# Kernel tuning notes

Measured on AMD Instinct MI355X. Metric: run time of the kernel, lower is better.

The kernel has to match this reference:

```python
import jax, jax.numpy as jnp
import numpy as np

TOTAL_WORDS = 10000
EMBED_LEN = 100
SEQ_LEN = 80
BATCH = 2048
UNITS = 1024


def setup_inputs() -> dict:
    key = jax.random.key(0)
    ks = jax.random.split(key, 8)
    inputs = jax.random.randint(ks[0], (BATCH, SEQ_LEN), 0, TOTAL_WORDS)
    s = 0.02
    emb = jax.random.normal(ks[1], (TOTAL_WORDS, EMBED_LEN), jnp.float32) * s
    W0 = jax.random.normal(ks[2], (EMBED_LEN, 4 * UNITS), jnp.float32) * s
    U0 = jax.random.normal(ks[3], (UNITS, 4 * UNITS), jnp.float32) * s
    b0 = jnp.zeros((4 * UNITS,), jnp.float32)
    W1 = jax.random.normal(ks[4], (UNITS, 4 * UNITS), jnp.float32) * s
    U1 = jax.random.normal(ks[5], (UNITS, 4 * UNITS), jnp.float32) * s
    b1 = jnp.zeros((4 * UNITS,), jnp.float32)
    fcW = jax.random.normal(ks[6], (UNITS, 1), jnp.float32) * s
    fcb = jnp.zeros((1,), jnp.float32)
    return {"inputs": inputs, "emb": emb, "W0": W0, "U0": U0, "b0": b0,
            "W1": W1, "U1": U1, "b1": b1, "fcW": fcW, "fcb": fcb}


def _lstm_step(x, h, c, W, U, b):
    # Keras LSTMCell gate order: i, f, g(candidate), o
    z = x @ W + h @ U + b  # [B, 4*units]
    i, f, g, o = jnp.split(z, 4, axis=-1)
    i = jax.nn.sigmoid(i)
    f = jax.nn.sigmoid(f)
    g = jnp.tanh(g)
    o = jax.nn.sigmoid(o)
    c_new = f * c + i * g
    h_new = o * jnp.tanh(c_new)
    return h_new, c_new


def reference(inputs, emb, W0, U0, b0, W1, U1, b1, fcW, fcb):
    x = emb[inputs]                      # [B, T, E]
    xs = jnp.transpose(x, (1, 0, 2))     # [T, B, E] for scan over time
    B = inputs.shape[0]
    U = U0.shape[0]
    init = (jnp.zeros((B, U), x.dtype), jnp.zeros((B, U), x.dtype),
            jnp.zeros((B, U), x.dtype), jnp.zeros((B, U), x.dtype))

    def step(carry, xt):
        h0, c0, h1, c1 = carry
        h0, c0 = _lstm_step(xt, h0, c0, W0, U0, b0)
        h1, c1 = _lstm_step(h0, h1, c1, W1, U1, b1)
        return (h0, c0, h1, c1), None

    (h0, c0, h1, c1), _ = jax.lax.scan(step, init, xs)
    logits = h1 @ fcW + fcb              # [B, 1]
    return jax.nn.sigmoid(logits)
```

## Files before the change

### kernel.cpp

```cpp
#include <hip/hip_runtime.h>

#define DEVI __device__ __forceinline__

typedef __attribute__((ext_vector_type(4))) float f4;
typedef long long i64t;

DEVI unsigned char f2fp8(float x) {
  int p = __builtin_amdgcn_cvt_pk_fp8_f32(x, x, 0, false);
  return (unsigned char)(p & 0xff);
}
DEVI float fp82f(unsigned char b) {
  return __builtin_amdgcn_cvt_f32_fp8((int)b, 0);
}
DEVI float sigmoidf_(float x) { return 1.f / (1.f + __expf(-x)); }
DEVI float tanhf_(float x) {
  float ax = fabsf(x);
  float e = __expf(-2.f * ax);
  float t = (1.f - e) / (1.f + e);
  return x < 0.f ? -t : t;
}

#define GLDS16(g, l) __builtin_amdgcn_global_load_lds( \
    (const __attribute__((address_space(1))) void*)(g), \
    (__attribute__((address_space(3))) void*)(l), 16, 0, 0)

#define SCALE_UP 64.0f
#define SCALE_DN (1.0f / 4096.0f)


__global__ void k_conv_emb(const float* __restrict__ emb, unsigned char* __restrict__ ep) {
  int i = blockIdx.x * 256 + threadIdx.x;
  if (i >= 10000 * 128) return;
  int r = i >> 7, c = i & 127;
  ep[i] = (c < 100) ? f2fp8(emb[r * 100 + c] * SCALE_UP) : (unsigned char)0;
}

DEVI int permn(int n) {
  int g = n >> 10, u = n & 1023;
  return (u >> 5) * 128 + ((u >> 4) & 1) * 64 + g * 16 + (u & 15);
}
DEVI int kswz(int klog, int row) {
  return (klog & ~63) | (((((klog >> 3) & 7) ^ ((row >> 1) & 7))) << 3) | (klog & 7);
}

__global__ void k_conv_w0(const float* __restrict__ W0, const float* __restrict__ U0,
                          unsigned char* __restrict__ WT) {
  int i = blockIdx.x * 256 + threadIdx.x;
  if (i >= 4096 * 1152) return;
  int n = i / 1152, k = i - n * 1152;
  float v;
  if (k < 100) v = W0[k * 4096 + n];
  else if (k < 128) v = 0.f;
  else v = U0[(k - 128) * 4096 + n];
  int np = permn(n);
  WT[(size_t)np * 1152 + kswz(k, np)] = f2fp8(v * SCALE_UP);
}

__global__ void k_conv_w1(const float* __restrict__ W1, const float* __restrict__ U1,
                          unsigned char* __restrict__ WT) {
  int i = blockIdx.x * 256 + threadIdx.x;
  if (i >= 4096 * 2048) return;
  int n = i >> 11, k = i & 2047;
  float v = (k < 1024) ? W1[k * 4096 + n] : U1[(k - 1024) * 4096 + n];
  int np = permn(n);
  WT[(size_t)np * 2048 + kswz(k, np)] = f2fp8(v * SCALE_UP);
}


template<int K1, int KTOT, bool GATHER>
DEVI void lstm_body(int tile, char* smem,
    const unsigned char* __restrict__ src1,
    const unsigned char* __restrict__ src2,
    const int* __restrict__ idx, int t,
    const unsigned char* __restrict__ WT,
    const float* __restrict__ bias,
    float* __restrict__ cbuf,
    unsigned char* __restrict__ hout)
{
  const int tid = threadIdx.x;
  const int bn = tile & 31;
  const int bm = tile >> 5;
  const int m0 = bm * 256;
  const int n0 = bn * 128;

  const int lr = tid >> 2;
  const int c16 = (tid & 3) * 16;
  const int csw = (((tid & 3) ^ ((tid >> 3) & 3))) * 16;

  const unsigned char* g1[2];
  if (GATHER) {
#pragma unroll
    for (int p = 0; p < 2; ++p) {
      int w = idx[(m0 + p * 128 + lr) * 80 + t];
      g1[p] = src1 + (size_t)w * K1 + csw;
    }
  }

  const unsigned char* wbase = WT + (size_t)(n0 + lr) * KTOT + c16;
  const unsigned char* a1b[2];
  const unsigned char* a2b[2];
#pragma unroll
  for (int p = 0; p < 2; ++p) {
    size_t row = (size_t)(m0 + p * 128 + lr);
    a1b[p] = src1 + row * 1024 + c16;
    a2b[p] = src2 + row * 1024 + c16 - K1;
  }

  char* const LA0 = smem;
  char* const LB0 = smem + 16384;
  char* const LA1 = smem + 24576;
  char* const LB1 = smem + 40960;

  auto stage = [&](int kb, char* la, char* lb) {
    const int kc = kb * 64;
    if (GATHER && kc < K1) {
#pragma unroll
      for (int p = 0; p < 2; ++p)
        GLDS16(g1[p] + kc, la + p * 8192 + tid * 16);
    } else {
#pragma unroll
      for (int p = 0; p < 2; ++p) {
        const unsigned char* g = (!GATHER && kc < K1) ? a1b[p] + kc
                                                      : a2b[p] + kc;
        GLDS16(g, la + p * 8192 + tid * 16);
      }
    }
    GLDS16(wbase + kc, lb + tid * 16);
  };

  const int lane = tid & 63;
  const int wv = tid >> 6;
  const int wm = wv >> 1;
  const int wn = wv & 1;
  const int cl = lane & 15;
  const int qd = lane >> 4;
  const int qh = qd >> 1, qb = qd & 1;
  const int g8s = (cl >> 1) & 7;
  const int ko8_0 = ((0 + qd) ^ g8s) << 3;
  const int ko8_1 = ((4 + qd) ^ g8s) << 3;
  const int g4s = (cl >> 1) & 3;
  const int ko16_0 = ((qh ^ g4s) << 4) + qb * 8;
  const int ko16_1 = (((2 + qh) ^ g4s) << 4) + qb * 8;

  f4 acc[4][4];
  const f4 fz = {0.f, 0.f, 0.f, 0.f};
#pragma unroll
  for (int a = 0; a < 4; ++a)
#pragma unroll
    for (int b = 0; b < 4; ++b) acc[a][b] = fz;

  auto compute = [&](char* la, char* lb, int koA0, int koA1) {
#pragma unroll
    for (int kk = 0; kk < 2; ++kk) {
      const int koA = kk ? koA1 : koA0;
      const int koB = kk ? ko8_1 : ko8_0;
      i64t af[4], bfr[4];
#pragma unroll
      for (int mi = 0; mi < 4; ++mi)
        af[mi] = *(const i64t*)(la + (wm * 64 + mi * 16 + cl) * 64 + koA);
#pragma unroll
      for (int j = 0; j < 4; ++j)
        bfr[j] = *(const i64t*)(lb + (wn * 64 + j * 16 + cl) * 64 + koB);
#pragma unroll
      for (int mi = 0; mi < 4; ++mi)
#pragma unroll
        for (int j = 0; j < 4; ++j)
          acc[mi][j] = __builtin_amdgcn_mfma_f32_16x16x32_fp8_fp8(
              af[mi], bfr[j], acc[mi][j], 0, 0, 0);
    }
  };

  stage(0, LA0, LB0);

  constexpr int NKB = KTOT / 64;
  static_assert(NKB % 2 == 0, "K-loop unroll-2 requires even NKB");
#pragma unroll 1
  for (int kbp = 0; kbp < NKB / 2; ++kbp) {
    const int kb0 = kbp * 2;
    __syncthreads();
    stage(kb0 + 1, LA1, LB1);
    {
      const bool A16 = GATHER && (kb0 * 64) < K1;
      compute(LA0, LB0, A16 ? ko16_0 : ko8_0, A16 ? ko16_1 : ko8_1);
    }
    __syncthreads();
    if (kb0 + 2 < NKB) stage(kb0 + 2, LA0, LB0);
    {
      const bool A16 = GATHER && ((kb0 + 1) * 64) < K1;
      compute(LA1, LB1, A16 ? ko16_0 : ko8_0, A16 ? ko16_1 : ko8_1);
    }
  }

  const int u = bn * 32 + wn * 16 + cl;
  const int uhi = u & ~63;
  const int uc8 = (u >> 3) & 7;
  const int ulo = u & 7;
  const float bi = bias[u];
  const float bff = bias[1024 + u];
  const float bg = bias[2048 + u];
  const float bo = bias[3072 + u];
#pragma unroll
  for (int mi = 0; mi < 4; ++mi) {
    int mbase = m0 + wm * 64 + mi * 16 + qd * 4;
#pragma unroll
    for (int r = 0; r < 4; ++r) {
      int m = mbase + r;
      int fm = (qd * 2 + (r >> 1)) & 7;
      int hcol = uhi | ((uc8 ^ fm) << 3) | ulo;
      float gi = sigmoidf_(acc[mi][0][r] * SCALE_DN + bi);
      float gf = sigmoidf_(acc[mi][1][r] * SCALE_DN + bff);
      float gg = tanhf_(acc[mi][2][r] * SCALE_DN + bg);
      float go = sigmoidf_(acc[mi][3][r] * SCALE_DN + bo);
      size_t coff = (size_t)m * 1024 + u;
      float cn = gf * cbuf[coff] + gi * gg;
      cbuf[coff] = cn;
      hout[(size_t)m * 1024 + hcol] = f2fp8(go * tanhf_(cn) * SCALE_UP);
    }
  }
}

__global__ __launch_bounds__(512, 4) void k_step(
    int mode,
    const unsigned char* embp, const unsigned char* h0in,
    const int* idx, int t,
    const unsigned char* WT0, const float* b0, float* c0, unsigned char* h0out,
    const unsigned char* h0prev, const unsigned char* h1in,
    const unsigned char* WT1, const float* b1, float* c1, unsigned char* h1out)
{
  extern __shared__ char smem[];
  const int blk = blockIdx.x;
  int tile;
  bool isL0;
  if (mode == 1) {
    int s = blk >> 3;
    isL0 = ((s & 1) ^ (s >> 5)) != 0;
    tile = (blk & 7) * 32 + (s & 31);
  } else {
    tile = (blk & 7) * 32 + (blk >> 3);
    isL0 = (mode == 0);
  }
  if (isL0)
    lstm_body<128, 1152, true>(tile, smem, embp, h0in, idx, t,
                               WT0, b0, c0, h0out);
  else
    lstm_body<1024, 2048, false>(tile, smem, h0prev, h1in, nullptr, 0,
                                 WT1, b1, c1, h1out);
}


__global__ void k_fc(const unsigned char* __restrict__ h1,
                     const float* __restrict__ fcW, const float* __restrict__ fcb,
                     float* __restrict__ out) {
  int wv = threadIdx.x >> 6;
  int lane = threadIdx.x & 63;
  int row = blockIdx.x * 4 + wv;
  if (row >= 2048) return;
  const unsigned char* hr = h1 + (size_t)row * 1024;
  const int f = (row >> 1) & 7;
  float s = 0.f;
  for (int k = lane; k < 1024; k += 64) {
    int ks = (k & ~63) | ((((k >> 3) & 7) ^ f) << 3) | (k & 7);
    s += fp82f(hr[ks]) * fcW[k];
  }
#pragma unroll
  for (int off = 32; off > 0; off >>= 1) s += __shfl_down(s, off);
  if (lane == 0) out[row] = sigmoidf_(s * (1.0f / SCALE_UP) + fcb[0]);
}


extern "C" void kernel_launch(void* const* d_in, const int* in_sizes, int n_in,
                              void* d_out, int out_size, void* d_ws, size_t ws_size,
                              hipStream_t stream) {
  const int*   idx = (const int*)d_in[0];
  const float* emb = (const float*)d_in[1];
  const float* W0  = (const float*)d_in[2];
  const float* U0  = (const float*)d_in[3];
  const float* b0  = (const float*)d_in[4];
  const float* W1  = (const float*)d_in[5];
  const float* U1  = (const float*)d_in[6];
  const float* b1  = (const float*)d_in[7];
  const float* fcW = (const float*)d_in[8];
  const float* fcb = (const float*)d_in[9];
  float* out = (float*)d_out;

  char* ws = (char*)d_ws;
  unsigned char* embp = (unsigned char*)(ws);
  unsigned char* WT0  = (unsigned char*)(ws + 1280000);
  unsigned char* WT1  = (unsigned char*)(ws + 5998592);
  unsigned char* h0b[2] = {(unsigned char*)(ws + 14387200),
                           (unsigned char*)(ws + 16484352)};
  unsigned char* h1b[2] = {(unsigned char*)(ws + 18581504),
                           (unsigned char*)(ws + 20678656)};
  float* c0 = (float*)(ws + 22775808);
  float* c1 = (float*)(ws + 31164416);

  hipMemsetAsync(ws + 14387200, 0, 25165824, stream);

  k_conv_emb<<<5000, 256, 0, stream>>>(emb, embp);
  k_conv_w0<<<18432, 256, 0, stream>>>(W0, U0, WT0);
  k_conv_w1<<<32768, 256, 0, stream>>>(W1, U1, WT1);

  k_step<<<256, 512, 49152, stream>>>(0, embp, h0b[1], idx, 0,
                                      WT0, b0, c0, h0b[0],
                                      nullptr, nullptr, WT1, b1, c1, nullptr);
  for (int t = 1; t < 80; ++t) {
    k_step<<<512, 512, 49152, stream>>>(1, embp, h0b[(t + 1) & 1], idx, t,
                                        WT0, b0, c0, h0b[t & 1],
                                        h0b[(t - 1) & 1], h1b[t & 1],
                                        WT1, b1, c1, h1b[(t + 1) & 1]);
  }
  k_step<<<256, 512, 49152, stream>>>(2, nullptr, nullptr, nullptr, 0,
                                      WT0, b0, c0, nullptr,
                                      h0b[1], h1b[0], WT1, b1, c1, h1b[1]);

  k_fc<<<512, 256, 0, stream>>>(h1b[1], fcW, fcb, out);
}
```

Measured before the change: 4.028 ms.

## Halve M tile to 128 and run both LSTM layers per block sequentially

Changes each block from a 256x128 tile of one layer to a 128x128 tile that computes layer 0 and then layer 1 in sequence within the same block. Shared memory per block drops from 48KB to 32KB and the accumulator count halves, which frees registers and LDS. The aim is better occupancy and a uniform per-block workload. In exchange each weight tile is loaded for twice as many M tiles, which lowers data reuse and raises weight traffic.

```diff
diff --git a/kernel.cpp b/kernel.cpp
--- a/kernel.cpp
+++ b/kernel.cpp
@@ -68,7 +68,7 @@
 
 
 template<int K1, int KTOT, bool GATHER>
-DEVI void lstm_body(int tile, char* smem,
+DEVI void lstm_phase(int m0, int n0, char* smem,
     const unsigned char* __restrict__ src1,
     const unsigned char* __restrict__ src2,
     const int* __restrict__ idx, int t,
@@ -78,52 +78,33 @@
     unsigned char* __restrict__ hout)
 {
   const int tid = threadIdx.x;
-  const int bn = tile & 31;
-  const int bm = tile >> 5;
-  const int m0 = bm * 256;
-  const int n0 = bn * 128;
 
   const int lr = tid >> 2;
   const int c16 = (tid & 3) * 16;
   const int csw = (((tid & 3) ^ ((tid >> 3) & 3))) * 16;
 
-  const unsigned char* g1[2];
+  const unsigned char* g1 = nullptr;
   if (GATHER) {
-#pragma unroll
-    for (int p = 0; p < 2; ++p) {
-      int w = idx[(m0 + p * 128 + lr) * 80 + t];
-      g1[p] = src1 + (size_t)w * K1 + csw;
-    }
+    int w = idx[(m0 + lr) * 80 + t];
+    g1 = src1 + (size_t)w * K1 + csw;
   }
 
   const unsigned char* wbase = WT + (size_t)(n0 + lr) * KTOT + c16;
-  const unsigned char* a1b[2];
-  const unsigned char* a2b[2];
-#pragma unroll
-  for (int p = 0; p < 2; ++p) {
-    size_t row = (size_t)(m0 + p * 128 + lr);
-    a1b[p] = src1 + row * 1024 + c16;
-    a2b[p] = src2 + row * 1024 + c16 - K1;
-  }
+  const unsigned char* a1b = src1 + (size_t)(m0 + lr) * 1024 + c16;
+  const unsigned char* a2b = src2 + (size_t)(m0 + lr) * 1024 + c16 - K1;
 
   char* const LA0 = smem;
-  char* const LB0 = smem + 16384;
-  char* const LA1 = smem + 24576;
-  char* const LB1 = smem + 40960;
+  char* const LB0 = smem + 8192;
+  char* const LA1 = smem + 16384;
+  char* const LB1 = smem + 24576;
 
   auto stage = [&](int kb, char* la, char* lb) {
     const int kc = kb * 64;
     if (GATHER && kc < K1) {
-#pragma unroll
-      for (int p = 0; p < 2; ++p)
-        GLDS16(g1[p] + kc, la + p * 8192 + tid * 16);
+      GLDS16(g1 + kc, la + tid * 16);
     } else {
-#pragma unroll
-      for (int p = 0; p < 2; ++p) {
-        const unsigned char* g = (!GATHER && kc < K1) ? a1b[p] + kc
-                                                      : a2b[p] + kc;
-        GLDS16(g, la + p * 8192 + tid * 16);
-      }
+      const unsigned char* g = (!GATHER && kc < K1) ? a1b + kc : a2b + kc;
+      GLDS16(g, la + tid * 16);
     }
     GLDS16(wbase + kc, lb + tid * 16);
   };
@@ -142,10 +123,10 @@
   const int ko16_0 = ((qh ^ g4s) << 4) + qb * 8;
   const int ko16_1 = (((2 + qh) ^ g4s) << 4) + qb * 8;
 
-  f4 acc[4][4];
+  f4 acc[2][4];
   const f4 fz = {0.f, 0.f, 0.f, 0.f};
 #pragma unroll
-  for (int a = 0; a < 4; ++a)
+  for (int a = 0; a < 2; ++a)
 #pragma unroll
     for (int b = 0; b < 4; ++b) acc[a][b] = fz;
 
@@ -154,15 +135,15 @@
     for (int kk = 0; kk < 2; ++kk) {
       const int koA = kk ? koA1 : koA0;
       const int koB = kk ? ko8_1 : ko8_0;
-      i64t af[4], bfr[4];
-#pragma unroll
-      for (int mi = 0; mi < 4; ++mi)
-        af[mi] = *(const i64t*)(la + (wm * 64 + mi * 16 + cl) * 64 + koA);
+      i64t af[2], bfr[4];
+#pragma unroll
+      for (int mi = 0; mi < 2; ++mi)
+        af[mi] = *(const i64t*)(la + (wm * 32 + mi * 16 + cl) * 64 + koA);
 #pragma unroll
       for (int j = 0; j < 4; ++j)
         bfr[j] = *(const i64t*)(lb + (wn * 64 + j * 16 + cl) * 64 + koB);
 #pragma unroll
-      for (int mi = 0; mi < 4; ++mi)
+      for (int mi = 0; mi < 2; ++mi)
 #pragma unroll
         for (int j = 0; j < 4; ++j)
           acc[mi][j] = __builtin_amdgcn_mfma_f32_16x16x32_fp8_fp8(
@@ -191,7 +172,7 @@
     }
   }
 
-  const int u = bn * 32 + wn * 16 + cl;
+  const int u = n0 / 4 + wn * 16 + cl;
   const int uhi = u & ~63;
   const int uc8 = (u >> 3) & 7;
   const int ulo = u & 7;
@@ -200,8 +181,8 @@
   const float bg = bias[2048 + u];
   const float bo = bias[3072 + u];
 #pragma unroll
-  for (int mi = 0; mi < 4; ++mi) {
-    int mbase = m0 + wm * 64 + mi * 16 + qd * 4;
+  for (int mi = 0; mi < 2; ++mi) {
+    int mbase = m0 + wm * 32 + mi * 16 + qd * 4;
 #pragma unroll
     for (int r = 0; r < 4; ++r) {
       int m = mbase + r;
@@ -229,22 +210,14 @@
 {
   extern __shared__ char smem[];
   const int blk = blockIdx.x;
-  int tile;
-  bool isL0;
-  if (mode == 1) {
-    int s = blk >> 3;
-    isL0 = ((s & 1) ^ (s >> 5)) != 0;
-    tile = (blk & 7) * 32 + (s & 31);
-  } else {
-    tile = (blk & 7) * 32 + (blk >> 3);
-    isL0 = (mode == 0);
-  }
-  if (isL0)
-    lstm_body<128, 1152, true>(tile, smem, embp, h0in, idx, t,
-                               WT0, b0, c0, h0out);
-  else
-    lstm_body<1024, 2048, false>(tile, smem, h0prev, h1in, nullptr, 0,
-                                 WT1, b1, c1, h1out);
+  const int m0 = (blk >> 5) * 128;
+  const int n0 = (blk & 31) * 128;
+  if (mode != 2)
+    lstm_phase<128, 1152, true>(m0, n0, smem, embp, h0in, idx, t,
+                                WT0, b0, c0, h0out);
+  if (mode != 0)
+    lstm_phase<1024, 2048, false>(m0, n0, smem, h0prev, h1in, nullptr, 0,
+                                  WT1, b1, c1, h1out);
 }
 
 
@@ -300,16 +273,16 @@
   k_conv_w0<<<18432, 256, 0, stream>>>(W0, U0, WT0);
   k_conv_w1<<<32768, 256, 0, stream>>>(W1, U1, WT1);
 
-  k_step<<<256, 512, 49152, stream>>>(0, embp, h0b[1], idx, 0,
+  k_step<<<512, 512, 32768, stream>>>(0, embp, h0b[1], idx, 0,
                                       WT0, b0, c0, h0b[0],
                                       nullptr, nullptr, WT1, b1, c1, nullptr);
   for (int t = 1; t < 80; ++t) {
-    k_step<<<512, 512, 49152, stream>>>(1, embp, h0b[(t + 1) & 1], idx, t,
+    k_step<<<512, 512, 32768, stream>>>(1, embp, h0b[(t + 1) & 1], idx, t,
                                         WT0, b0, c0, h0b[t & 1],
                                         h0b[(t - 1) & 1], h1b[t & 1],
                                         WT1, b1, c1, h1b[(t + 1) & 1]);
   }
-  k_step<<<256, 512, 49152, stream>>>(2, nullptr, nullptr, nullptr, 0,
+  k_step<<<512, 512, 32768, stream>>>(2, nullptr, nullptr, nullptr, 0,
                                       WT0, b0, c0, nullptr,
                                       h0b[1], h1b[0], WT1, b1, c1, h1b[1]);
 
```

After: 3.914 ms. 2.8% less time.
